# Kernel optimization log

Hardware: AMD Instinct MI355X
Metric: run time of the kernel (lower is better)

Reference implementation:

```python
import jax, jax.numpy as jnp
import numpy as np

B, P, H = 32768, 128, 64

def setup_inputs() -> dict:
    key = jax.random.key(0)
    ks = jax.random.split(key, 6)
    planet_xy = jax.random.normal(ks[0], (B, P, 2), dtype=jnp.float32)
    planet_m = jax.random.uniform(ks[1], (P,), dtype=jnp.float32)
    ast_xy = jax.random.normal(ks[2], (B, 2), dtype=jnp.float32)
    W1 = jax.random.normal(ks[3], (4, H), dtype=jnp.float32) * 0.5
    b1 = jnp.zeros((H,), dtype=jnp.float32)
    W2 = jax.random.normal(ks[4], (H, H), dtype=jnp.float32) * 0.125
    b2 = jnp.zeros((H,), dtype=jnp.float32)
    return {"planet_xy": planet_xy, "planet_m": planet_m, "ast_xy": ast_xy,
            "W1": W1, "b1": b1, "W2": W2, "b2": b2}

def reference(planet_xy, planet_m, ast_xy, W1, b1, W2, b2):
    # d: (B, P, 2) broadcast difference planet - asteroid
    d = planet_xy - ast_xy[:, None, :]
    dist2 = jnp.sum(d * d, axis=-1) + 1e-6            # (B, P)
    invdist = 1.0 / jnp.sqrt(dist2)                   # (B, P)
    m = jnp.broadcast_to(planet_m[None, :], dist2.shape)  # (B, P)
    feats = jnp.concatenate([d, invdist[..., None], m[..., None]], axis=-1)  # (B, P, 4)
    h = jax.nn.relu(jnp.einsum('bpf,fh->bph', feats, W1) + b1)  # (B, P, H)
    msg = jax.nn.relu(jnp.einsum('bph,hk->bpk', h, W2) + b2)    # (B, P, H)
    return msg.sum(axis=1)                             # (B, H)
```

## Files before the change

### kernel.cpp

```cpp
#include <hip/hip_runtime.h>
#include <hip/hip_fp16.h>

#define NP    128
#define NH    64
#define ITERS 4
#define WPB   4

typedef __attribute__((ext_vector_type(8))) _Float16 f16x8;
typedef __attribute__((ext_vector_type(4))) _Float16 f16x4;
typedef __attribute__((ext_vector_type(2))) __fp16  hf16x2;
typedef __attribute__((ext_vector_type(4))) float f32x4;

union FragK16 { f16x4 v; unsigned int u[2]; };
union FragK32 { f16x8 v; unsigned int u[4]; };

__device__ __forceinline__ unsigned int pack_pkrtz(float a, float b) {
    hf16x2 t = __builtin_amdgcn_cvt_pkrtz(a, b);
    return __builtin_bit_cast(unsigned int, t);
}

__device__ __forceinline__ unsigned int relu2_pk(unsigned int u) {
    hf16x2 h = __builtin_bit_cast(hf16x2, u);
    h = __builtin_elementwise_max(h, (hf16x2)(__fp16)0.f);
    return __builtin_bit_cast(unsigned int, h);
}

__global__ void __launch_bounds__(256, 2) gnn_wave(
    const float* __restrict__ planet_xy,
    const float* __restrict__ planet_m,
    const float* __restrict__ ast_xy,
    const float* __restrict__ W1,
    const float* __restrict__ b1,
    const float* __restrict__ W2,
    const float* __restrict__ b2,
    float* __restrict__ out)
{
    const int tid  = threadIdx.x;
    const int wv   = tid >> 6;
    const int lane = tid & 63;
    const int q    = lane >> 4;
    const int lm   = lane & 15;
    const bool q0  = (q == 0);
    const bool q1  = (q == 1);

    FragK16 w1f[4];
    #pragma unroll
    for (int mt = 0; mt < 4; mt++) {
        const int m = 16 * mt + lm;
        float wa = W1[0 * NH + m], wb = W1[1 * NH + m];
        float wc = W1[2 * NH + m], wd = W1[3 * NH + m];
        float be = b1[m];
        w1f[mt].u[0] = q0 ? pack_pkrtz(wa, wb) : (q1 ? pack_pkrtz(be, 0.f) : 0u);
        w1f[mt].u[1] = q0 ? pack_pkrtz(wc, wd) : 0u;
    }

    FragK32 w2b[4][2];
    #pragma unroll
    for (int np = 0; np < 4; np++)
        #pragma unroll
        for (int kk = 0; kk < 2; kk++) {
            const int n = 16 * np + lm;
            const int k0 = 32 * kk + 4 * q;
            const int k1 = 32 * kk + 16 + 4 * q;
            w2b[np][kk].u[0] = pack_pkrtz(W2[(k0 + 0) * NH + n], W2[(k0 + 1) * NH + n]);
            w2b[np][kk].u[1] = pack_pkrtz(W2[(k0 + 2) * NH + n], W2[(k0 + 3) * NH + n]);
            w2b[np][kk].u[2] = pack_pkrtz(W2[(k1 + 0) * NH + n], W2[(k1 + 1) * NH + n]);
            w2b[np][kk].u[3] = pack_pkrtz(W2[(k1 + 2) * NH + n], W2[(k1 + 3) * NH + n]);
        }

    f32x4 b2f[4];
    #pragma unroll
    for (int np = 0; np < 4; np++) {
        const float bv = b2[16 * np + lm];
        b2f[np] = (f32x4){bv, bv, bv, bv};
    }

    float pmv[8];
    #pragma unroll
    for (int i = 0; i < 8; i++)
        pmv[i] = planet_m[16 * i + lm];

    const unsigned int bf0_const = q1 ? pack_pkrtz(1.f, 0.f) : 0u;
    const f32x4 zf = (f32x4){0.f, 0.f, 0.f, 0.f};

    FragK16 onesA;
    onesA.u[0] = 0x3C003C00u;
    onesA.u[1] = 0x3C003C00u;

    int b = (blockIdx.x * WPB + wv) * ITERS;

    for (int it = 0; it < ITERS; ++it, ++b) {
        const float2 axy = *(const float2*)&ast_xy[2 * b];
        float2 pxy[8];
        #pragma unroll
        for (int i = 0; i < 8; i++)
            pxy[i] = *(const float2*)&planet_xy[((size_t)b * NP + 16 * i + lm) * 2];

        f32x4 redD[4];
        #pragma unroll
        for (int np = 0; np < 4; np++)
            redD[np] = zf;

        #pragma unroll
        for (int mi = 0; mi < 8; ++mi) {
            float dx = pxy[mi].x - axy.x, dy = pxy[mi].y - axy.y;
            float inv = __builtin_amdgcn_rsqf(fmaf(dx, dx, fmaf(dy, dy, 1e-6f)));
            FragK16 bf;
            bf.u[0] = q0 ? pack_pkrtz(dx, dy)        : bf0_const;
            bf.u[1] = q0 ? pack_pkrtz(inv, pmv[mi])  : 0u;

            FragK16 hb[4];
            #pragma unroll
            for (int mt = 0; mt < 4; mt++) {
                f32x4 c = __builtin_amdgcn_mfma_f32_16x16x16f16(w1f[mt].v, bf.v, zf, 0, 0, 0);
                hb[mt].u[0] = relu2_pk(pack_pkrtz(c[0], c[1]));
                hb[mt].u[1] = relu2_pk(pack_pkrtz(c[2], c[3]));
            }

            FragK32 hA[2];
            #pragma unroll
            for (int kk = 0; kk < 2; kk++) {
                hA[kk].u[0] = hb[2 * kk + 0].u[0];
                hA[kk].u[1] = hb[2 * kk + 0].u[1];
                hA[kk].u[2] = hb[2 * kk + 1].u[0];
                hA[kk].u[3] = hb[2 * kk + 1].u[1];
            }

            #pragma unroll
            for (int np = 0; np < 4; np++) {
                f32x4 acc = __builtin_amdgcn_mfma_f32_16x16x32_f16(hA[0].v, w2b[np][0].v, b2f[np], 0, 0, 0);
                acc = __builtin_amdgcn_mfma_f32_16x16x32_f16(hA[1].v, w2b[np][1].v, acc, 0, 0, 0);

                FragK16 mf;
                mf.u[0] = relu2_pk(pack_pkrtz(acc[0], acc[1]));
                mf.u[1] = relu2_pk(pack_pkrtz(acc[2], acc[3]));

                redD[np] = __builtin_amdgcn_mfma_f32_16x16x16f16(onesA.v, mf.v, redD[np], 0, 0, 0);
            }
        }

        float v = q0 ? redD[0][0]
                : q1 ? redD[1][0]
                : (q == 2) ? redD[2][0] : redD[3][0];
        out[(size_t)b * NH + lane] = v;
    }
}

extern "C" void kernel_launch(void* const* d_in, const int* in_sizes, int n_in,
                              void* d_out, int out_size, void* d_ws, size_t ws_size,
                              hipStream_t stream) {
    const float* planet_xy = (const float*)d_in[0];
    const float* planet_m  = (const float*)d_in[1];
    const float* ast_xy    = (const float*)d_in[2];
    const float* W1        = (const float*)d_in[3];
    const float* b1        = (const float*)d_in[4];
    const float* W2        = (const float*)d_in[5];
    const float* b2        = (const float*)d_in[6];
    float* outp            = (float*)d_out;

    const int B = in_sizes[2] / 2;
    const int batches_per_block = WPB * ITERS;
    const int grid = (B + batches_per_block - 1) / batches_per_block;

    gnn_wave<<<grid, 256, 0, stream>>>(planet_xy, planet_m, ast_xy, W1, b1, W2, b2, outp);
}
```

Baseline: 121.0 us.

## Software-prefetch next batch's planet positions and double ITERS per wave

Result: slower. 128.2 us (+5.9%).

```diff
diff --git a/kernel.cpp b/kernel.cpp
--- a/kernel.cpp
+++ b/kernel.cpp
@@ -3,7 +3,7 @@
 
 #define NP    128
 #define NH    64
-#define ITERS 4
+#define ITERS 8
 #define WPB   4
 
 typedef __attribute__((ext_vector_type(8))) _Float16 f16x8;
@@ -33,7 +33,8 @@
     const float* __restrict__ b1,
     const float* __restrict__ W2,
     const float* __restrict__ b2,
-    float* __restrict__ out)
+    float* __restrict__ out,
+    int Btot)
 {
     const int tid  = threadIdx.x;
     const int wv   = tid >> 6;
@@ -75,10 +76,10 @@
         b2f[np] = (f32x4){bv, bv, bv, bv};
     }
 
-    float pmv[8];
+    unsigned int pmh[4];
     #pragma unroll
-    for (int i = 0; i < 8; i++)
-        pmv[i] = planet_m[16 * i + lm];
+    for (int i = 0; i < 4; i++)
+        pmh[i] = pack_pkrtz(planet_m[32 * i + lm], planet_m[32 * i + 16 + lm]);
 
     const unsigned int bf0_const = q1 ? pack_pkrtz(1.f, 0.f) : 0u;
     const f32x4 zf = (f32x4){0.f, 0.f, 0.f, 0.f};
@@ -89,12 +90,16 @@
 
     int b = (blockIdx.x * WPB + wv) * ITERS;
 
+    float2 axy = *(const float2*)&ast_xy[2 * b];
+    float2 pxy[8];
+    #pragma unroll
+    for (int i = 0; i < 8; i++)
+        pxy[i] = *(const float2*)&planet_xy[((size_t)b * NP + 16 * i + lm) * 2];
+
+    #pragma unroll 1
     for (int it = 0; it < ITERS; ++it, ++b) {
-        const float2 axy = *(const float2*)&ast_xy[2 * b];
-        float2 pxy[8];
-        #pragma unroll
-        for (int i = 0; i < 8; i++)
-            pxy[i] = *(const float2*)&planet_xy[((size_t)b * NP + 16 * i + lm) * 2];
+        const int bn = (b + 1 < Btot) ? b + 1 : b;
+        const float2 axN = *(const float2*)&ast_xy[2 * bn];
 
         f32x4 redD[4];
         #pragma unroll
@@ -103,27 +108,25 @@
 
         #pragma unroll
         for (int mi = 0; mi < 8; ++mi) {
-            float dx = pxy[mi].x - axy.x, dy = pxy[mi].y - axy.y;
+            const float2 p = pxy[mi];
+            pxy[mi] = *(const float2*)&planet_xy[((size_t)bn * NP + 16 * mi + lm) * 2];
+
+            float dx = p.x - axy.x, dy = p.y - axy.y;
             float inv = __builtin_amdgcn_rsqf(fmaf(dx, dx, fmaf(dy, dy, 1e-6f)));
+            unsigned int invp = pack_pkrtz(inv, 0.f);
+            unsigned int pmsel = (mi & 1)
+                ? ((pmh[mi >> 1] & 0xFFFF0000u) | invp)
+                : ((pmh[mi >> 1] << 16) | invp);
             FragK16 bf;
-            bf.u[0] = q0 ? pack_pkrtz(dx, dy)        : bf0_const;
-            bf.u[1] = q0 ? pack_pkrtz(inv, pmv[mi])  : 0u;
+            bf.u[0] = q0 ? pack_pkrtz(dx, dy) : bf0_const;
+            bf.u[1] = q0 ? pmsel : 0u;
 
-            FragK16 hb[4];
+            FragK32 hA[2];
             #pragma unroll
             for (int mt = 0; mt < 4; mt++) {
                 f32x4 c = __builtin_amdgcn_mfma_f32_16x16x16f16(w1f[mt].v, bf.v, zf, 0, 0, 0);
-                hb[mt].u[0] = relu2_pk(pack_pkrtz(c[0], c[1]));
-                hb[mt].u[1] = relu2_pk(pack_pkrtz(c[2], c[3]));
-            }
-
-            FragK32 hA[2];
-            #pragma unroll
-            for (int kk = 0; kk < 2; kk++) {
-                hA[kk].u[0] = hb[2 * kk + 0].u[0];
-                hA[kk].u[1] = hb[2 * kk + 0].u[1];
-                hA[kk].u[2] = hb[2 * kk + 1].u[0];
-                hA[kk].u[3] = hb[2 * kk + 1].u[1];
+                hA[mt >> 1].u[2 * (mt & 1) + 0] = relu2_pk(pack_pkrtz(c[0], c[1]));
+                hA[mt >> 1].u[2 * (mt & 1) + 1] = relu2_pk(pack_pkrtz(c[2], c[3]));
             }
 
             #pragma unroll
@@ -138,6 +141,8 @@
                 redD[np] = __builtin_amdgcn_mfma_f32_16x16x16f16(onesA.v, mf.v, redD[np], 0, 0, 0);
             }
         }
+
+        axy = axN;
 
         float v = q0 ? redD[0][0]
                 : q1 ? redD[1][0]
@@ -162,5 +167,5 @@
     const int batches_per_block = WPB * ITERS;
     const int grid = (B + batches_per_block - 1) / batches_per_block;
 
-    gnn_wave<<<grid, 256, 0, stream>>>(planet_xy, planet_m, ast_xy, W1, b1, W2, b2, outp);
+    gnn_wave<<<grid, 256, 0, stream>>>(planet_xy, planet_m, ast_xy, W1, b1, W2, b2, outp, B);
 }
```

## Software-pipeline planet loads and layer-1 MFMAs across iterations

Applied to the files above, without the earlier changes.

Result: slower. 123.6 us (+2.1%).

```diff
diff --git a/kernel.cpp b/kernel.cpp
--- a/kernel.cpp
+++ b/kernel.cpp
@@ -89,55 +89,80 @@
 
     int b = (blockIdx.x * WPB + wv) * ITERS;
 
+    float2 axy = *(const float2*)&ast_xy[2 * b];
+    float2 pxy[8];
+    #pragma unroll
+    for (int i = 0; i < 8; i++)
+        pxy[i] = *(const float2*)&planet_xy[((size_t)b * NP + 16 * i + lm) * 2];
+
+    #pragma unroll 1
     for (int it = 0; it < ITERS; ++it, ++b) {
-        const float2 axy = *(const float2*)&ast_xy[2 * b];
-        float2 pxy[8];
-        #pragma unroll
-        for (int i = 0; i < 8; i++)
-            pxy[i] = *(const float2*)&planet_xy[((size_t)b * NP + 16 * i + lm) * 2];
+        const int bn = (it + 1 < ITERS) ? b + 1 : b;
+        const float* pnext = planet_xy + ((size_t)bn * NP + lm) * 2;
+
+        float2 axN = axy;
 
         f32x4 redD[4];
         #pragma unroll
         for (int np = 0; np < 4; np++)
             redD[np] = zf;
 
+        f32x4 c[4];
+        {
+            float dx = pxy[0].x - axy.x, dy = pxy[0].y - axy.y;
+            float inv = __builtin_amdgcn_rsqf(fmaf(dx, dx, fmaf(dy, dy, 1e-6f)));
+            FragK16 bf;
+            bf.u[0] = q0 ? pack_pkrtz(dx, dy)       : bf0_const;
+            bf.u[1] = q0 ? pack_pkrtz(inv, pmv[0])  : 0u;
+            #pragma unroll
+            for (int mt = 0; mt < 4; mt++)
+                c[mt] = __builtin_amdgcn_mfma_f32_16x16x16f16(w1f[mt].v, bf.v, zf, 0, 0, 0);
+        }
+
         #pragma unroll
         for (int mi = 0; mi < 8; ++mi) {
-            float dx = pxy[mi].x - axy.x, dy = pxy[mi].y - axy.y;
-            float inv = __builtin_amdgcn_rsqf(fmaf(dx, dx, fmaf(dy, dy, 1e-6f)));
-            FragK16 bf;
-            bf.u[0] = q0 ? pack_pkrtz(dx, dy)        : bf0_const;
-            bf.u[1] = q0 ? pack_pkrtz(inv, pmv[mi])  : 0u;
-
-            FragK16 hb[4];
+            FragK32 hA[2];
             #pragma unroll
             for (int mt = 0; mt < 4; mt++) {
-                f32x4 c = __builtin_amdgcn_mfma_f32_16x16x16f16(w1f[mt].v, bf.v, zf, 0, 0, 0);
-                hb[mt].u[0] = relu2_pk(pack_pkrtz(c[0], c[1]));
-                hb[mt].u[1] = relu2_pk(pack_pkrtz(c[2], c[3]));
+                hA[mt >> 1].u[2 * (mt & 1) + 0] = relu2_pk(pack_pkrtz(c[mt][0], c[mt][1]));
+                hA[mt >> 1].u[2 * (mt & 1) + 1] = relu2_pk(pack_pkrtz(c[mt][2], c[mt][3]));
             }
 
-            FragK32 hA[2];
-            #pragma unroll
-            for (int kk = 0; kk < 2; kk++) {
-                hA[kk].u[0] = hb[2 * kk + 0].u[0];
-                hA[kk].u[1] = hb[2 * kk + 0].u[1];
-                hA[kk].u[2] = hb[2 * kk + 1].u[0];
-                hA[kk].u[3] = hb[2 * kk + 1].u[1];
+            if (mi < 7) {
+                float dx = pxy[mi + 1].x - axy.x, dy = pxy[mi + 1].y - axy.y;
+                float inv = __builtin_amdgcn_rsqf(fmaf(dx, dx, fmaf(dy, dy, 1e-6f)));
+                FragK16 bf;
+                bf.u[0] = q0 ? pack_pkrtz(dx, dy)            : bf0_const;
+                bf.u[1] = q0 ? pack_pkrtz(inv, pmv[mi + 1])  : 0u;
+                #pragma unroll
+                for (int mt = 0; mt < 4; mt++)
+                    c[mt] = __builtin_amdgcn_mfma_f32_16x16x16f16(w1f[mt].v, bf.v, zf, 0, 0, 0);
             }
 
+            pxy[mi] = *(const float2*)(pnext + 32 * mi);
+            if (mi == 5)
+                axN = *(const float2*)&ast_xy[2 * bn];
+
+            f32x4 acc[4];
+            #pragma unroll
+            for (int np = 0; np < 4; np++)
+                acc[np] = __builtin_amdgcn_mfma_f32_16x16x32_f16(hA[0].v, w2b[np][0].v, b2f[np], 0, 0, 0);
+            #pragma unroll
+            for (int np = 0; np < 4; np++)
+                acc[np] = __builtin_amdgcn_mfma_f32_16x16x32_f16(hA[1].v, w2b[np][1].v, acc[np], 0, 0, 0);
+
+            FragK16 mf[4];
             #pragma unroll
             for (int np = 0; np < 4; np++) {
-                f32x4 acc = __builtin_amdgcn_mfma_f32_16x16x32_f16(hA[0].v, w2b[np][0].v, b2f[np], 0, 0, 0);
-                acc = __builtin_amdgcn_mfma_f32_16x16x32_f16(hA[1].v, w2b[np][1].v, acc, 0, 0, 0);
+                mf[np].u[0] = relu2_pk(pack_pkrtz(acc[np][0], acc[np][1]));
+                mf[np].u[1] = relu2_pk(pack_pkrtz(acc[np][2], acc[np][3]));
+            }
+            #pragma unroll
+            for (int np = 0; np < 4; np++)
+                redD[np] = __builtin_amdgcn_mfma_f32_16x16x16f16(onesA.v, mf[np].v, redD[np], 0, 0, 0);
+        }
 
-                FragK16 mf;
-                mf.u[0] = relu2_pk(pack_pkrtz(acc[0], acc[1]));
-                mf.u[1] = relu2_pk(pack_pkrtz(acc[2], acc[3]));
-
-                redD[np] = __builtin_amdgcn_mfma_f32_16x16x16f16(onesA.v, mf.v, redD[np], 0, 0, 0);
-            }
-        }
+        axy = axN;
 
         float v = q0 ? redD[0][0]
                 : q1 ? redD[1][0]
```

## Replace ones-MFMA planet reduction with fp32 VALU sums and cross-lane shuffles

Applied to the files above, without the earlier changes.

After: 131.5 us. 8.7% more time.

```diff
diff --git a/kernel.cpp b/kernel.cpp
--- a/kernel.cpp
+++ b/kernel.cpp
@@ -25,7 +25,7 @@
     return __builtin_bit_cast(unsigned int, h);
 }
 
-__global__ void __launch_bounds__(256, 2) gnn_wave(
+__global__ void __launch_bounds__(256, 3) gnn_wave(
     const float* __restrict__ planet_xy,
     const float* __restrict__ planet_m,
     const float* __restrict__ ast_xy,
@@ -83,12 +83,9 @@
     const unsigned int bf0_const = q1 ? pack_pkrtz(1.f, 0.f) : 0u;
     const f32x4 zf = (f32x4){0.f, 0.f, 0.f, 0.f};
 
-    FragK16 onesA;
-    onesA.u[0] = 0x3C003C00u;
-    onesA.u[1] = 0x3C003C00u;
-
     int b = (blockIdx.x * WPB + wv) * ITERS;
 
+    #pragma unroll 1
     for (int it = 0; it < ITERS; ++it, ++b) {
         const float2 axy = *(const float2*)&ast_xy[2 * b];
         float2 pxy[8];
@@ -96,10 +93,7 @@
         for (int i = 0; i < 8; i++)
             pxy[i] = *(const float2*)&planet_xy[((size_t)b * NP + 16 * i + lm) * 2];
 
-        f32x4 redD[4];
-        #pragma unroll
-        for (int np = 0; np < 4; np++)
-            redD[np] = zf;
+        f32x4 vsum = zf;
 
         #pragma unroll
         for (int mi = 0; mi < 8; ++mi) {
@@ -109,39 +103,34 @@
             bf.u[0] = q0 ? pack_pkrtz(dx, dy)        : bf0_const;
             bf.u[1] = q0 ? pack_pkrtz(inv, pmv[mi])  : 0u;
 
-            FragK16 hb[4];
+            FragK32 hA[2];
             #pragma unroll
             for (int mt = 0; mt < 4; mt++) {
                 f32x4 c = __builtin_amdgcn_mfma_f32_16x16x16f16(w1f[mt].v, bf.v, zf, 0, 0, 0);
-                hb[mt].u[0] = relu2_pk(pack_pkrtz(c[0], c[1]));
-                hb[mt].u[1] = relu2_pk(pack_pkrtz(c[2], c[3]));
-            }
-
-            FragK32 hA[2];
-            #pragma unroll
-            for (int kk = 0; kk < 2; kk++) {
-                hA[kk].u[0] = hb[2 * kk + 0].u[0];
-                hA[kk].u[1] = hb[2 * kk + 0].u[1];
-                hA[kk].u[2] = hb[2 * kk + 1].u[0];
-                hA[kk].u[3] = hb[2 * kk + 1].u[1];
+                hA[mt >> 1].u[2 * (mt & 1) + 0] = relu2_pk(pack_pkrtz(c[0], c[1]));
+                hA[mt >> 1].u[2 * (mt & 1) + 1] = relu2_pk(pack_pkrtz(c[2], c[3]));
             }
 
             #pragma unroll
             for (int np = 0; np < 4; np++) {
                 f32x4 acc = __builtin_amdgcn_mfma_f32_16x16x32_f16(hA[0].v, w2b[np][0].v, b2f[np], 0, 0, 0);
                 acc = __builtin_amdgcn_mfma_f32_16x16x32_f16(hA[1].v, w2b[np][1].v, acc, 0, 0, 0);
-
-                FragK16 mf;
-                mf.u[0] = relu2_pk(pack_pkrtz(acc[0], acc[1]));
-                mf.u[1] = relu2_pk(pack_pkrtz(acc[2], acc[3]));
-
-                redD[np] = __builtin_amdgcn_mfma_f32_16x16x16f16(onesA.v, mf.v, redD[np], 0, 0, 0);
+                acc = __builtin_elementwise_max(acc, zf);
+                vsum[np] += (acc[0] + acc[1]) + (acc[2] + acc[3]);
             }
         }
 
-        float v = q0 ? redD[0][0]
-                : q1 ? redD[1][0]
-                : (q == 2) ? redD[2][0] : redD[3][0];
+        #pragma unroll
+        for (int np = 0; np < 4; np++) {
+            float s = vsum[np];
+            s += __shfl_xor(s, 16, 64);
+            s += __shfl_xor(s, 32, 64);
+            vsum[np] = s;
+        }
+
+        float v = q0 ? vsum[0]
+                : q1 ? vsum[1]
+                : (q == 2) ? vsum[2] : vsum[3];
         out[(size_t)b * NH + lane] = v;
     }
 }
```
